# Performance work log

Measured on AMD Instinct MI355X. Metric: run time of the kernel, lower is better.

## Reference

```python
import jax, jax.numpy as jnp
import numpy as np

B, O, Q, QD, SG = 8, 1024, 2048, 1024, 1200

def setup_inputs() -> dict:
    key = jax.random.key(0)
    k1, k2, k3 = jax.random.split(key, 3)
    query_in = jax.random.normal(k1, (B, O, QD), dtype=jnp.float32)
    context_in = jax.random.normal(k2, (B, Q, SG), dtype=jnp.float32)
    # linear_in.weight initialized uniform(-0.1, 0.1) in the torch module
    W = jax.random.uniform(k3, (SG, QD), dtype=jnp.float32, minval=-0.1, maxval=0.1)
    return {"query_in": query_in, "context_in": context_in, "W": W}

def reference(query_in, context_in, W):
    # general attention: project query from query_dim -> sg_dim (no bias)
    query = jnp.einsum('boq,sq->bos', query_in, W)          # [B, O, SG]
    scores = jnp.einsum('bos,bqs->boq', query, context_in)   # [B, O, Q] (unscaled)
    weights = jax.nn.softmax(scores, axis=-1)                # [B, O, Q]
    mix = jnp.einsum('boq,bqs->bos', weights, context_in)    # [B, O, SG]
    return (mix, weights)
```

## Files before the change

kernel.cpp:

```cpp
#include <hip/hip_runtime.h>
#include <hip/hip_bf16.h>


typedef _Float16 half8 __attribute__((ext_vector_type(8)));
typedef _Float16 half4v __attribute__((ext_vector_type(4)));
typedef float    f32x4 __attribute__((ext_vector_type(4)));

#define AS1C(p) ((const __attribute__((address_space(1))) void*)(p))
#define AS3(p)  ((__attribute__((address_space(3))) void*)(p))

#define WAITV8() do { asm volatile("s_waitcnt vmcnt(8)" ::: "memory"); __builtin_amdgcn_sched_barrier(0); } while(0)
#define WAITV4() do { asm volatile("s_waitcnt vmcnt(4)" ::: "memory"); __builtin_amdgcn_sched_barrier(0); } while(0)
#define WAITV0() do { asm volatile("s_waitcnt vmcnt(0)" ::: "memory"); __builtin_amdgcn_sched_barrier(0); } while(0)
#define WAITL0() do { asm volatile("s_waitcnt lgkmcnt(0)" ::: "memory"); __builtin_amdgcn_sched_barrier(0); } while(0)


__device__ __forceinline__ void stage_tile(const _Float16* __restrict__ X, _Float16* s,
                                           int t, long row0, long rowmax, int ld, int k0)
{
#pragma unroll
    for (int j = 0; j < 2; ++j) {
        const int L = t + 256 * j;
        const int r = L >> 2;
        const int slot = L & 3;
        const int koff = slot ^ ((r >> 1) & 3);
        long grow = row0 + r; if (grow > rowmax) grow = rowmax;
        const _Float16* src = X + grow * (long)ld + k0 + koff * 8;
        _Float16* dst = s + (long)((t & ~63) + 256 * j) * 8;
        __builtin_amdgcn_global_load_lds(AS1C(src), AS3(dst), 16, 0, 0);
    }
}

__device__ __forceinline__ void stage256(const _Float16* __restrict__ X, _Float16* s,
                                         int t, long row0, int ld, int k0)
{
#pragma unroll
    for (int j = 0; j < 2; ++j) {
        const int L = t + 512 * j;
        const int r = L >> 2;
        const int slot = L & 3;
        const int koff = slot ^ ((r >> 1) & 3);
        const _Float16* src = X + (row0 + r) * (long)ld + k0 + koff * 8;
        _Float16* dst = s + (long)((t & ~63) + 512 * j) * 8;
        __builtin_amdgcn_global_load_lds(AS1C(src), AS3(dst), 16, 0, 0);
    }
}

__device__ __forceinline__ half8 frag(const _Float16* s, int row, int kslot)
{
    return *(const half8*)(s + row * 32 + ((kslot ^ ((row >> 1) & 3)) << 3));
}

#define T2K 38
__global__ __launch_bounds__(512, 2) void gemm2_8p(
    const _Float16* __restrict__ Ahp, const _Float16* __restrict__ Alp,
    const _Float16* __restrict__ Bhp, const _Float16* __restrict__ Blp,
    float* __restrict__ Cf)
{
    const int t = threadIdx.x;
    const int bz = blockIdx.z;
    const _Float16* A_h = Ahp + bz * (1024L * 1216);
    const _Float16* A_l = Alp + bz * (1024L * 1216);
    const _Float16* B_h = Bhp + bz * (2048L * 1216);
    const _Float16* B_l = Blp + bz * (2048L * 1216);

    __shared__ __align__(16) _Float16 slots[4][2][256 * 32];

    const long row0 = (long)blockIdx.y * 256;
    const long col0 = (long)blockIdx.x * 256;

    const int wid = t >> 6, lane = t & 63;
    const int wr = wid >> 2, wc = wid & 3;
    const int fr = lane & 15, kslot = lane >> 4;

    f32x4 acc[8][4];
#pragma unroll
    for (int i = 0; i < 8; ++i)
#pragma unroll
        for (int j = 0; j < 4; ++j) acc[i][j] = (f32x4){0.f, 0.f, 0.f, 0.f};

    stage256(A_h, &slots[0][0][0], t, row0, 1216, 0);
    stage256(B_h, &slots[0][1][0], t, col0, 1216, 0);
    stage256(A_l, &slots[1][0][0], t, row0, 1216, 0);
    stage256(B_l, &slots[1][1][0], t, col0, 1216, 0);
    stage256(A_h, &slots[2][0][0], t, row0, 1216, 32);
    stage256(B_h, &slots[2][1][0], t, col0, 1216, 32);

    for (int tt = 0; tt < T2K; ++tt) {
        const int s0 = (2 * tt) & 3, s1 = (2 * tt + 1) & 3;

        if (tt < T2K - 1) WAITV8(); else WAITV4();
        __builtin_amdgcn_s_barrier();

        half8 a_h[8], b_h[4];
#pragma unroll
        for (int i = 0; i < 8; ++i) a_h[i] = frag(&slots[s0][0][0], wr * 128 + i * 16 + fr, kslot);
#pragma unroll
        for (int i = 0; i < 4; ++i) b_h[i] = frag(&slots[s0][1][0], wc * 64 + i * 16 + fr, kslot);

        if (tt < T2K - 1) {
            const int k0 = (tt + 1) * 32, sl = (2 * tt + 3) & 3;
            stage256(A_l, &slots[sl][0][0], t, row0, 1216, k0);
            stage256(B_l, &slots[sl][1][0], t, col0, 1216, k0);
        }
        __builtin_amdgcn_s_barrier();
        WAITL0();
        __builtin_amdgcn_s_setprio(1);
#pragma unroll
        for (int mi = 0; mi < 8; ++mi)
#pragma unroll
            for (int ni = 0; ni < 4; ++ni)
                acc[mi][ni] = __builtin_amdgcn_mfma_f32_16x16x32_f16(a_h[mi], b_h[ni], acc[mi][ni], 0, 0, 0);
        __builtin_amdgcn_s_setprio(0);

        if (tt < T2K - 1) WAITV8(); else WAITV0();
        __builtin_amdgcn_s_barrier();

        half8 a_l[8], b_l[4];
#pragma unroll
        for (int i = 0; i < 8; ++i) a_l[i] = frag(&slots[s1][0][0], wr * 128 + i * 16 + fr, kslot);
#pragma unroll
        for (int i = 0; i < 4; ++i) b_l[i] = frag(&slots[s1][1][0], wc * 64 + i * 16 + fr, kslot);

        if (tt < T2K - 2) {
            const int k0 = (tt + 2) * 32, sl = (2 * tt + 4) & 3;
            stage256(A_h, &slots[sl][0][0], t, row0, 1216, k0);
            stage256(B_h, &slots[sl][1][0], t, col0, 1216, k0);
        }
        __builtin_amdgcn_s_barrier();
        WAITL0();
        __builtin_amdgcn_s_setprio(1);
#pragma unroll
        for (int mi = 0; mi < 8; ++mi)
#pragma unroll
            for (int ni = 0; ni < 4; ++ni) {
                acc[mi][ni] = __builtin_amdgcn_mfma_f32_16x16x32_f16(a_h[mi], b_l[ni], acc[mi][ni], 0, 0, 0);
                acc[mi][ni] = __builtin_amdgcn_mfma_f32_16x16x32_f16(a_l[mi], b_h[ni], acc[mi][ni], 0, 0, 0);
            }
        __builtin_amdgcn_s_setprio(0);
    }

    const int r4 = (lane >> 4) * 4;
    float* C = Cf + bz * (1024L * 2048);
#pragma unroll
    for (int mi = 0; mi < 8; ++mi)
#pragma unroll
        for (int ni = 0; ni < 4; ++ni) {
            const long colg = col0 + wc * 64 + ni * 16 + fr;
#pragma unroll
            for (int r = 0; r < 4; ++r) {
                const long rowg = row0 + wr * 128 + mi * 16 + r4 + r;
                C[rowg * 2048 + colg] = acc[mi][ni][r];
            }
        }
}

template<bool SPLIT, bool OUT16>
__global__ __launch_bounds__(256) void gemm16(
    const _Float16* __restrict__ Ah, const _Float16* __restrict__ Al,
    const _Float16* __restrict__ Bh, const _Float16* __restrict__ Bl,
    float* __restrict__ Cf, _Float16* __restrict__ Ch, _Float16* __restrict__ Cl,
    int N, int K, int lda, int ldb, int ldc,
    long sA, long sB, long sC)
{
    const int t = threadIdx.x;
    const int bz = blockIdx.z;
    const _Float16* A_h = Ah + bz * sA;
    const _Float16* B_h = Bh + bz * sB;
    const _Float16* A_l = SPLIT ? (Al + bz * sA) : nullptr;
    const _Float16* B_l = SPLIT ? (Bl + bz * sB) : nullptr;

    __shared__ __align__(16) _Float16 sAh[2][128 * 32];
    __shared__ __align__(16) _Float16 sBh[2][128 * 32];
    __shared__ __align__(16) _Float16 sAl[SPLIT ? 2 : 1][SPLIT ? 128 * 32 : 8];
    __shared__ __align__(16) _Float16 sBl[SPLIT ? 2 : 1][SPLIT ? 128 * 32 : 8];

    const long row0 = (long)blockIdx.y * 128;
    const int  col0 = blockIdx.x * 128;

    const int wid = t >> 6, lane = t & 63;
    const int wm = (wid >> 1) * 64, wn = (wid & 1) * 64;
    const int fr = lane & 15, kslot = lane >> 4;

    f32x4 acc[4][4];
#pragma unroll
    for (int i = 0; i < 4; ++i)
#pragma unroll
        for (int j = 0; j < 4; ++j) acc[i][j] = (f32x4){0.f, 0.f, 0.f, 0.f};

    stage_tile(A_h, sAh[0], t, row0, row0 + 127, lda, 0);
    stage_tile(B_h, sBh[0], t, col0, N - 1, ldb, 0);
    if (SPLIT) {
        stage_tile(A_l, sAl[0], t, row0, row0 + 127, lda, 0);
        stage_tile(B_l, sBl[0], t, col0, N - 1, ldb, 0);
    }
    __syncthreads();

    int cur = 0;
    for (int k0 = 0; k0 < K; k0 += 32) {
        if (k0 + 32 < K) {
            const int nxt = cur ^ 1, kn = k0 + 32;
            stage_tile(A_h, sAh[nxt], t, row0, row0 + 127, lda, kn);
            stage_tile(B_h, sBh[nxt], t, col0, N - 1, ldb, kn);
            if (SPLIT) {
                stage_tile(A_l, sAl[nxt], t, row0, row0 + 127, lda, kn);
                stage_tile(B_l, sBl[nxt], t, col0, N - 1, ldb, kn);
            }
        }

        half8 a_h[4], b_h[4], a_l[4], b_l[4];
#pragma unroll
        for (int i = 0; i < 4; ++i) {
            a_h[i] = frag(sAh[cur], wm + i * 16 + fr, kslot);
            b_h[i] = frag(sBh[cur], wn + i * 16 + fr, kslot);
            if (SPLIT) {
                a_l[i] = frag(sAl[cur], wm + i * 16 + fr, kslot);
                b_l[i] = frag(sBl[cur], wn + i * 16 + fr, kslot);
            }
        }
#pragma unroll
        for (int mi = 0; mi < 4; ++mi)
#pragma unroll
            for (int ni = 0; ni < 4; ++ni) {
                acc[mi][ni] = __builtin_amdgcn_mfma_f32_16x16x32_f16(a_h[mi], b_h[ni], acc[mi][ni], 0, 0, 0);
                if (SPLIT) {
                    acc[mi][ni] = __builtin_amdgcn_mfma_f32_16x16x32_f16(a_h[mi], b_l[ni], acc[mi][ni], 0, 0, 0);
                    acc[mi][ni] = __builtin_amdgcn_mfma_f32_16x16x32_f16(a_l[mi], b_h[ni], acc[mi][ni], 0, 0, 0);
                }
            }

        __syncthreads();
        cur ^= 1;
    }

    const int r4 = (lane >> 4) * 4;
    float* C_f = OUT16 ? nullptr : (Cf + bz * sC);
#pragma unroll
    for (int mi = 0; mi < 4; ++mi)
#pragma unroll
        for (int ni = 0; ni < 4; ++ni) {
            const int colg = col0 + wn + ni * 16 + fr;
#pragma unroll
            for (int r = 0; r < 4; ++r) {
                const long rowg = row0 + wm + mi * 16 + r4 + r;
                const float v = acc[mi][ni][r];
                if (OUT16) {
                    if (colg < ldc) {
                        const float vv = (colg < N) ? v : 0.f;
                        const _Float16 hi = (_Float16)vv;
                        const _Float16 lo = (_Float16)(vv - (float)hi);
                        Ch[rowg * ldc + colg] = hi;
                        Cl[rowg * ldc + colg] = lo;
                    }
                } else {
                    if (colg < N) C_f[rowg * (long)ldc + colg] = v;
                }
            }
        }
}

__global__ __launch_bounds__(256) void qw_cvt(
    const float* __restrict__ Q, _Float16* __restrict__ QH, _Float16* __restrict__ QL,
    const float* __restrict__ Wt, _Float16* __restrict__ WH, _Float16* __restrict__ WL)
{
    const long NQ = 8192L * 1024 / 4;
    const long NT = NQ + 1200L * 1024 / 4;
    for (long i = (long)blockIdx.x * 256 + threadIdx.x; i < NT; i += (long)gridDim.x * 256) {
        const float* src; _Float16 *dh, *dl; long j;
        if (i < NQ) { j = i; src = Q; dh = QH; dl = QL; }
        else        { j = i - NQ; src = Wt; dh = WH; dl = WL; }
        float4 v = *(const float4*)(src + j * 4);
        const _Float16 h0 = (_Float16)v.x, h1 = (_Float16)v.y, h2 = (_Float16)v.z, h3 = (_Float16)v.w;
        const _Float16 l0 = (_Float16)(v.x - (float)h0), l1 = (_Float16)(v.y - (float)h1);
        const _Float16 l2 = (_Float16)(v.z - (float)h2), l3 = (_Float16)(v.w - (float)h3);
        *(half4v*)(dh + j * 4) = (half4v){h0, h1, h2, h3};
        *(half4v*)(dl + j * 4) = (half4v){l0, l1, l2, l3};
    }
}

__global__ __launch_bounds__(256) void ctx_prep(const float* __restrict__ X,
    _Float16* __restrict__ H, _Float16* __restrict__ L, _Float16* __restrict__ T)
{
    const int b = blockIdx.z;
    const float* Xb = X + (long)b * 2048 * 1200;
    _Float16* Hb = H + (long)b * 2048 * 1216;
    _Float16* Lb = L + (long)b * 2048 * 1216;
    _Float16* Tb = T + (long)b * 1200 * 2048;
    __shared__ _Float16 tl[32][33];
    const int tx = threadIdx.x & 31, ty = threadIdx.x >> 5;
    const int s0 = blockIdx.x * 32, q0 = blockIdx.y * 32;
#pragma unroll
    for (int p = 0; p < 4; ++p) {
        const int q = q0 + ty + p * 8, s = s0 + tx;
        const float v = (s < 1200) ? Xb[(long)q * 1200 + s] : 0.f;
        const _Float16 hi = (_Float16)v;
        Hb[(long)q * 1216 + s] = hi;
        Lb[(long)q * 1216 + s] = (_Float16)(v - (float)hi);
        tl[tx][ty + p * 8] = hi;
    }
    __syncthreads();
#pragma unroll
    for (int p = 0; p < 4; ++p) {
        const int s = s0 + ty + p * 8;
        if (s < 1200) Tb[(long)s * 2048 + q0 + tx] = tl[ty + p * 8][tx];
    }
}

__global__ __launch_bounds__(256) void softmax_k(float* __restrict__ w, _Float16* __restrict__ w16)
{
    float* p = w + (long)blockIdx.x * 2048;
    half4v* p16 = (half4v*)(w16 + (long)blockIdx.x * 2048);
    const int t = threadIdx.x;
    float4 v0 = ((const float4*)p)[t];
    float4 v1 = ((const float4*)p)[t + 256];

    float m = fmaxf(fmaxf(fmaxf(v0.x, v0.y), fmaxf(v0.z, v0.w)),
                    fmaxf(fmaxf(v1.x, v1.y), fmaxf(v1.z, v1.w)));
#pragma unroll
    for (int off = 1; off < 64; off <<= 1) m = fmaxf(m, __shfl_xor(m, off));
    __shared__ float redm[4], reds[4];
    const int wave = t >> 6, lane = t & 63;
    if (lane == 0) redm[wave] = m;
    __syncthreads();
    m = fmaxf(fmaxf(redm[0], redm[1]), fmaxf(redm[2], redm[3]));

    float e[8];
    e[0] = __expf(v0.x - m); e[1] = __expf(v0.y - m);
    e[2] = __expf(v0.z - m); e[3] = __expf(v0.w - m);
    e[4] = __expf(v1.x - m); e[5] = __expf(v1.y - m);
    e[6] = __expf(v1.z - m); e[7] = __expf(v1.w - m);

    float s = ((e[0] + e[1]) + (e[2] + e[3])) + ((e[4] + e[5]) + (e[6] + e[7]));
#pragma unroll
    for (int off = 1; off < 64; off <<= 1) s += __shfl_xor(s, off);
    if (lane == 0) reds[wave] = s;
    __syncthreads();
    s = (reds[0] + reds[1]) + (reds[2] + reds[3]);

    const float inv = 1.0f / s;
    float o0 = e[0] * inv, o1 = e[1] * inv, o2 = e[2] * inv, o3 = e[3] * inv;
    float o4 = e[4] * inv, o5 = e[5] * inv, o6 = e[6] * inv, o7 = e[7] * inv;
    ((float4*)p)[t]       = make_float4(o0, o1, o2, o3);
    ((float4*)p)[t + 256] = make_float4(o4, o5, o6, o7);
    p16[t]       = (half4v){(_Float16)o0, (_Float16)o1, (_Float16)o2, (_Float16)o3};
    p16[t + 256] = (half4v){(_Float16)o4, (_Float16)o5, (_Float16)o6, (_Float16)o7};
}

extern "C" void kernel_launch(void* const* d_in, const int* in_sizes, int n_in,
                              void* d_out, int out_size, void* d_ws, size_t ws_size,
                              hipStream_t stream)
{
    const float* query_in = (const float*)d_in[0];
    const float* context  = (const float*)d_in[1];
    const float* W        = (const float*)d_in[2];

    float* mix    = (float*)d_out;
    float* scores = (float*)d_out + 9830400LL;

    _Float16* qh  = (_Float16*)d_ws;
    _Float16* ql  = qh  + 8388608;
    _Float16* wh  = ql  + 8388608;
    _Float16* wl  = wh  + 1228800;
    _Float16* ch  = wl  + 1228800;
    _Float16* cl  = ch  + 19922944;
    _Float16* ct  = cl  + 19922944;
    _Float16* qeh = ct  + 19660800;
    _Float16* qel = qeh + 9961472;
    _Float16* w16 = qel + 9961472;

    dim3 blk(256);

    qw_cvt<<<2400, blk, 0, stream>>>(query_in, qh, ql, W, wh, wl);
    ctx_prep<<<dim3(38, 64, 8), blk, 0, stream>>>(context, ch, cl, ct);

    gemm16<true, true><<<dim3(10, 64, 1), blk, 0, stream>>>(
        qh, ql, wh, wl, nullptr, qeh, qel,
        1200, 1024, 1024, 1024, 1216, 0, 0, 0);

    gemm2_8p<<<dim3(8, 4, 8), dim3(512), 0, stream>>>(qeh, qel, ch, cl, scores);

    softmax_k<<<dim3(8192), blk, 0, stream>>>(scores, w16);

    gemm16<false, false><<<dim3(10, 8, 8), blk, 0, stream>>>(
        w16, nullptr, ct, nullptr, mix, nullptr, nullptr,
        1200, 2048, 2048, 2048, 1200, 1024L * 2048, 1200L * 2048, 1024L * 1200);
}
```

Baseline: 521.3 us.

## Use three-slot async pipeline with explicit vmcnt waits in gemm16

Replaces the double-buffered hi/lo LDS staging in the generic fp16 GEMM with a three-slot ring buffer. In split mode the hi and lo halves are streamed as separate stages, and the hi fragments are kept in registers for the cross terms. Waits now use explicit vmcnt counts plus raw s_barrier instead of __syncthreads, which keeps up to two tiles of loads in flight. MFMA sections run at raised wave priority, and launch bounds request three blocks per CU. The aim is to hide global load latency; the cost is tight register pressure and waitcnt logic that depends on how many loads stage_tile issues.

```diff
diff --git a/kernel.cpp b/kernel.cpp
--- a/kernel.cpp
+++ b/kernel.cpp
@@ -156,7 +156,7 @@
 }
 
 template<bool SPLIT, bool OUT16>
-__global__ __launch_bounds__(256) void gemm16(
+__global__ __launch_bounds__(256, 3) void gemm8p(
     const _Float16* __restrict__ Ah, const _Float16* __restrict__ Al,
     const _Float16* __restrict__ Bh, const _Float16* __restrict__ Bl,
     float* __restrict__ Cf, _Float16* __restrict__ Ch, _Float16* __restrict__ Cl,
@@ -170,13 +170,12 @@
     const _Float16* A_l = SPLIT ? (Al + bz * sA) : nullptr;
     const _Float16* B_l = SPLIT ? (Bl + bz * sB) : nullptr;
 
-    __shared__ __align__(16) _Float16 sAh[2][128 * 32];
-    __shared__ __align__(16) _Float16 sBh[2][128 * 32];
-    __shared__ __align__(16) _Float16 sAl[SPLIT ? 2 : 1][SPLIT ? 128 * 32 : 8];
-    __shared__ __align__(16) _Float16 sBl[SPLIT ? 2 : 1][SPLIT ? 128 * 32 : 8];
+    __shared__ __align__(16) _Float16 slots[3][2][128 * 32];
 
     const long row0 = (long)blockIdx.y * 128;
-    const int  col0 = blockIdx.x * 128;
+    const long col0 = (long)blockIdx.x * 128;
+    const long rowAmax = row0 + 127;
+    const long rowBmax = N - 1;
 
     const int wid = t >> 6, lane = t & 63;
     const int wm = (wid >> 1) * 64, wn = (wid & 1) * 64;
@@ -188,49 +187,64 @@
 #pragma unroll
         for (int j = 0; j < 4; ++j) acc[i][j] = (f32x4){0.f, 0.f, 0.f, 0.f};
 
-    stage_tile(A_h, sAh[0], t, row0, row0 + 127, lda, 0);
-    stage_tile(B_h, sBh[0], t, col0, N - 1, ldb, 0);
-    if (SPLIT) {
-        stage_tile(A_l, sAl[0], t, row0, row0 + 127, lda, 0);
-        stage_tile(B_l, sBl[0], t, col0, N - 1, ldb, 0);
-    }
-    __syncthreads();
-
-    int cur = 0;
-    for (int k0 = 0; k0 < K; k0 += 32) {
-        if (k0 + 32 < K) {
-            const int nxt = cur ^ 1, kn = k0 + 32;
-            stage_tile(A_h, sAh[nxt], t, row0, row0 + 127, lda, kn);
-            stage_tile(B_h, sBh[nxt], t, col0, N - 1, ldb, kn);
+    const int KT = K >> 5;
+    const int G = SPLIT ? (KT << 1) : KT;
+
+#pragma unroll
+    for (int h = 0; h < 3; ++h) {
+        const int tn = SPLIT ? (h >> 1) : h;
+        const bool hi = SPLIT ? !(h & 1) : true;
+        stage_tile(hi ? A_h : A_l, &slots[h][0][0], t, row0, rowAmax, lda, tn * 32);
+        stage_tile(hi ? B_h : B_l, &slots[h][1][0], t, col0, rowBmax, ldb, tn * 32);
+    }
+
+    half8 a_hi[4], b_hi[4];
+    int sl = 0;
+    for (int g = 0; g < G; ++g) {
+        const int rem = G - 1 - g;
+        if (rem >= 2) WAITV8(); else if (rem == 1) WAITV4(); else WAITV0();
+        __builtin_amdgcn_s_barrier();
+
+        half8 a[4], b[4];
+#pragma unroll
+        for (int i = 0; i < 4; ++i) {
+            a[i] = frag(&slots[sl][0][0], wm + i * 16 + fr, kslot);
+            b[i] = frag(&slots[sl][1][0], wn + i * 16 + fr, kslot);
+        }
+        WAITL0();
+        __builtin_amdgcn_s_barrier();
+
+        if (g + 3 < G) {
+            const int gn = g + 3;
+            const int tn = SPLIT ? (gn >> 1) : gn;
+            const bool hi = SPLIT ? !(gn & 1) : true;
+            stage_tile(hi ? A_h : A_l, &slots[sl][0][0], t, row0, rowAmax, lda, tn * 32);
+            stage_tile(hi ? B_h : B_l, &slots[sl][1][0], t, col0, rowBmax, ldb, tn * 32);
+        }
+
+        __builtin_amdgcn_s_setprio(1);
+        if (!SPLIT || !(g & 1)) {
+#pragma unroll
+            for (int mi = 0; mi < 4; ++mi)
+#pragma unroll
+                for (int ni = 0; ni < 4; ++ni)
+                    acc[mi][ni] = __builtin_amdgcn_mfma_f32_16x16x32_f16(a[mi], b[ni], acc[mi][ni], 0, 0, 0);
             if (SPLIT) {
-                stage_tile(A_l, sAl[nxt], t, row0, row0 + 127, lda, kn);
-                stage_tile(B_l, sBl[nxt], t, col0, N - 1, ldb, kn);
+#pragma unroll
+                for (int i = 0; i < 4; ++i) { a_hi[i] = a[i]; b_hi[i] = b[i]; }
             }
-        }
-
-        half8 a_h[4], b_h[4], a_l[4], b_l[4];
-#pragma unroll
-        for (int i = 0; i < 4; ++i) {
-            a_h[i] = frag(sAh[cur], wm + i * 16 + fr, kslot);
-            b_h[i] = frag(sBh[cur], wn + i * 16 + fr, kslot);
-            if (SPLIT) {
-                a_l[i] = frag(sAl[cur], wm + i * 16 + fr, kslot);
-                b_l[i] = frag(sBl[cur], wn + i * 16 + fr, kslot);
-            }
-        }
-#pragma unroll
-        for (int mi = 0; mi < 4; ++mi)
-#pragma unroll
-            for (int ni = 0; ni < 4; ++ni) {
-                acc[mi][ni] = __builtin_amdgcn_mfma_f32_16x16x32_f16(a_h[mi], b_h[ni], acc[mi][ni], 0, 0, 0);
-                if (SPLIT) {
-                    acc[mi][ni] = __builtin_amdgcn_mfma_f32_16x16x32_f16(a_h[mi], b_l[ni], acc[mi][ni], 0, 0, 0);
-                    acc[mi][ni] = __builtin_amdgcn_mfma_f32_16x16x32_f16(a_l[mi], b_h[ni], acc[mi][ni], 0, 0, 0);
+        } else {
+#pragma unroll
+            for (int mi = 0; mi < 4; ++mi)
+#pragma unroll
+                for (int ni = 0; ni < 4; ++ni) {
+                    acc[mi][ni] = __builtin_amdgcn_mfma_f32_16x16x32_f16(a_hi[mi], b[ni], acc[mi][ni], 0, 0, 0);
+                    acc[mi][ni] = __builtin_amdgcn_mfma_f32_16x16x32_f16(a[mi], b_hi[ni], acc[mi][ni], 0, 0, 0);
                 }
-            }
-
-        __syncthreads();
-        cur ^= 1;
+        }
+        __builtin_amdgcn_s_setprio(0);
+
+        sl = (sl == 2) ? 0 : sl + 1;
     }
 
     const int r4 = (lane >> 4) * 4;
@@ -239,7 +253,7 @@
     for (int mi = 0; mi < 4; ++mi)
 #pragma unroll
         for (int ni = 0; ni < 4; ++ni) {
-            const int colg = col0 + wn + ni * 16 + fr;
+            const int colg = (int)col0 + wn + ni * 16 + fr;
 #pragma unroll
             for (int r = 0; r < 4; ++r) {
                 const long rowg = row0 + wm + mi * 16 + r4 + r;
@@ -373,7 +387,7 @@
     qw_cvt<<<2400, blk, 0, stream>>>(query_in, qh, ql, W, wh, wl);
     ctx_prep<<<dim3(38, 64, 8), blk, 0, stream>>>(context, ch, cl, ct);
 
-    gemm16<true, true><<<dim3(10, 64, 1), blk, 0, stream>>>(
+    gemm8p<true, true><<<dim3(10, 64, 1), blk, 0, stream>>>(
         qh, ql, wh, wl, nullptr, qeh, qel,
         1200, 1024, 1024, 1024, 1216, 0, 0, 0);
 
@@ -381,7 +395,7 @@
 
     softmax_k<<<dim3(8192), blk, 0, stream>>>(scores, w16);
 
-    gemm16<false, false><<<dim3(10, 8, 8), blk, 0, stream>>>(
+    gemm8p<false, false><<<dim3(10, 8, 8), blk, 0, stream>>>(
         w16, nullptr, ct, nullptr, mix, nullptr, nullptr,
         1200, 2048, 2048, 2048, 1200, 1024L * 2048, 1200L * 2048, 1024L * 1200);
 }
```

Result: slower. 822.9 us (+57.9%).
